# Optimization experiments

Hardware: AMD Instinct MI355X
Metric: run time of the kernel (lower is better)

Reference implementation:

```python
import jax, jax.numpy as jnp
import numpy as np

H = 4       # num_heads (forced == num_gates by reshape math in source)
G = 4       # num_gates
HID = 1024  # hidden_size
D = HID // H  # head_dim = 256
T = 512     # sequence length
B = 16      # batch


def setup_inputs() -> dict:
    key = jax.random.key(0)
    k1, k2, k3 = jax.random.split(key, 3)
    lim = 1.0 / np.sqrt(HID)
    # x holds pre-projected gate preactivations Wx: [T, B, 4*hidden]
    x = jax.random.normal(k1, (T, B, G * HID), dtype=jnp.float32) * 0.1
    recurrent_kernel = jax.random.uniform(k2, (H, D, G, D), dtype=jnp.float32, minval=-lim, maxval=lim)
    bias = jax.random.uniform(k3, (H, G, D), dtype=jnp.float32, minval=-lim, maxval=lim)
    return {"x": x, "recurrent_kernel": recurrent_kernel, "bias": bias}


def reference(x, recurrent_kernel, bias):
    # Reproduce the source's reshape chain (valid since H == G == 4):
    # rk: [H, D, G, D] -> permute(0,2,3,1) -> [H, G, D, D] -> reshape(H, D, H*D)
    rk1 = jnp.transpose(recurrent_kernel, (0, 2, 3, 1)).reshape(H, D, H * D)
    # transpose(1,2) -> [H, H*D, D] -> reshape(H, D, G*D)
    rk2 = jnp.swapaxes(rk1, 1, 2).reshape(H, D, G * D)
    bflat = bias.reshape(-1)  # head-major flatten, as in source
    Bsz = x.shape[1]
    zero = jnp.zeros((Bsz, HID), dtype=x.dtype)

    def step(carry, Wx_t):
        h, c, n, m = carry
        # Ry: [B,H,1,D] @ [1,H,D,G*D] -> [B,H,G*D] -> [B,H,G,D] -> [B,G,H,D] -> [B, G*HID]
        Ry = jnp.einsum('bhd,hdg->bhg', h.reshape(Bsz, H, D), rk2)
        Ry = Ry.reshape(Bsz, H, G, D).transpose(0, 2, 1, 3).reshape(Bsz, -1)
        raw = (Wx_t + Ry + bflat).reshape(Bsz, G, HID)
        iraw, fraw, zraw, oraw = raw[:, 0], raw[:, 1], raw[:, 2], raw[:, 3]
        logfplusm = m + jax.nn.log_sigmoid(fraw)
        # source: if all(n == 0): mnew = iraw else max(iraw, logfplusm)
        mnew = jnp.where(jnp.all(n == 0.0), iraw, jnp.maximum(iraw, logfplusm))
        ogate = jax.nn.sigmoid(oraw)
        igate = jnp.exp(iraw - mnew)
        fgate = jnp.exp(logfplusm - mnew)
        cnew = fgate * c + igate * jnp.tanh(zraw)
        nnew = fgate * h + igate  # faithful to source (uses hidden_state, not n)
        hnew = ogate * cnew / nnew
        return (hnew, cnew, nnew, mnew), hnew

    carry0 = (zero, zero, zero, zero)
    (hT, cT, nT, mT), outs = jax.lax.scan(step, carry0, x)
    # output = all_states[0][1:] (hidden over time), state = all_states[:, -1]
    final_state = jnp.stack((hT, cT, nT, mT), axis=0)
    return outs, final_state
```

## Files before the change

### kernel.cpp

```cpp
#include <hip/hip_runtime.h>
#include <hip/hip_fp16.h>
#include <stdint.h>


#define NTS 512
#define OUTS_ELEMS (NTS * 16 * 1024)

typedef _Float16 half2v __attribute__((ext_vector_type(2)));

__device__ __forceinline__ float fdot2f(uint32_t a, uint32_t b, float c) {
#if __has_builtin(__builtin_amdgcn_fdot2)
  union U { uint32_t u; half2v h; };
  U ua, ub; ua.u = a; ub.u = b;
  return __builtin_amdgcn_fdot2(ua.h, ub.h, c, false);
#else
  __half2 ha, hb;
  *(uint32_t*)&ha = a; *(uint32_t*)&hb = b;
  float2 fa = __half22float2(ha), fb = __half22float2(hb);
  return fmaf(fa.y, fb.y, fmaf(fa.x, fb.x, c));
#endif
}

__global__ void repack_weights(const float* __restrict__ rk,
                               uint32_t* __restrict__ wp) {
  int tid = blockIdx.x * 256 + threadIdx.x;
  int dd   = tid & 3;
  int lane = (tid >> 2) & 63;
  int m    = (tid >> 8) & 31;
  int w    = (tid >> 13) & 3;
  int hq   = tid >> 15;
  int head = hq >> 2, q4 = hq & 3;
  int n = m * 4 + dd;
  int g = n >> 5, p = n & 31;
  uint32_t word = 0;
  #pragma unroll
  for (int e = 0; e < 2; ++e) {
    int klo = 2 * p + e;
    float v = rk[head * 262144 + (klo * 4 + g) * 1024 + q4 * 256 + lane * 4 + w];
    word |= (uint32_t)__half_as_ushort(__float2half(v)) << (16 * e);
  }
  wp[tid] = word;
}

__global__ __launch_bounds__(256, 1) void slstm_main(
    const float* __restrict__ x, const float* __restrict__ bias,
    const uint32_t* __restrict__ wp, uint32_t* hex,
    float* __restrict__ out) {
  __shared__ __align__(16) unsigned short lh[4][64];
  __shared__ __align__(16) float4 pa[2][4][64];

  const int bid = blockIdx.x;
  const int xcd = bid & 7, yy = bid >> 3;
  const int q4 = yy & 3, ii = yy >> 2;
  const int cc = xcd * 8 + ii;
  const int b = cc >> 2, head = cc & 3;
  const int lane = threadIdx.x & 63, w = threadIdx.x >> 6;
  const int hq = head * 4 + q4;
  const int j_abs = q4 * 64 + lane;
  const bool is_pub = (w == 0);
  const bool is_own = (w == q4);
  const bool needs_gates = is_pub || is_own;

  uint32_t wr_[128];
  {
    const uint4* wp4 = (const uint4*)wp;
    int base = ((hq * 4 + w) * 32) * 64 + lane;
    #pragma unroll
    for (int mm = 0; mm < 32; ++mm) {
      uint4 v = wp4[base + mm * 64];
      wr_[mm * 4 + 0] = v.x; wr_[mm * 4 + 1] = v.y;
      wr_[mm * 4 + 2] = v.z; wr_[mm * 4 + 3] = v.w;
    }
  }

  float bg[4];
  #pragma unroll
  for (int g = 0; g < 4; ++g) bg[g] = bias[g * 1024 + head * 256 + j_abs];

  const int xoff0 = b * 4096 + head * 256 + j_abs;
  float xv[4] = {0.f, 0.f, 0.f, 0.f};
  if (needs_gates) {
    #pragma unroll
    for (int g = 0; g < 4; ++g) xv[g] = x[xoff0 + g * 1024];
  }

  const int rd_idx = cc * 256 + w * 64 + lane;
  const int wr_idx = cc * 256 + j_abs;
  const int out_off = b * 1024 + head * 256 + j_abs;

  float hs = 0.f, cs = 0.f, nns = 0.f, ms = 0.f;

  #pragma unroll 1
  for (int t = 0; t < NTS; ++t) {
    float A0 = 0.f, A1 = 0.f, A2 = 0.f, A3 = 0.f;
    float xn0 = 0.f, xn1 = 0.f, xn2 = 0.f, xn3 = 0.f;
    if (t > 0) {
      if (!is_own) {
        const uint32_t tg = (uint32_t)(t - 1);
        uint32_t* sp = hex + ((t - 1) & 1) * 16384 + rd_idx;
        uint32_t v; int spins = 0;
        for (;;) {
          v = __hip_atomic_load(sp, __ATOMIC_RELAXED, __HIP_MEMORY_SCOPE_AGENT);
          if (__all((v & 0xffffu) == tg) || ++spins > (1 << 15)) break;
        }
        lh[w][lane] = (unsigned short)(v >> 16);
      }
      if (needs_gates && t < NTS - 1) {
        int xo = xoff0 + (t + 1) * 65536;
        xn0 = x[xo]; xn1 = x[xo + 1024]; xn2 = x[xo + 2048]; xn3 = x[xo + 3072];
      }
      float a0 = 0.f, a1 = 0.f, a2 = 0.f, a3 = 0.f;
      {
        uint32_t hr[32];
        const float4* hp = (const float4*)&lh[w][0];
        #pragma unroll
        for (int f = 0; f < 8; ++f) {
          float4 fv = hp[f];
          hr[f * 4 + 0] = __float_as_uint(fv.x);
          hr[f * 4 + 1] = __float_as_uint(fv.y);
          hr[f * 4 + 2] = __float_as_uint(fv.z);
          hr[f * 4 + 3] = __float_as_uint(fv.w);
        }
        #pragma unroll
        for (int p = 0; p < 32; ++p) {
          uint32_t hh = hr[p];
          a0 = fdot2f(wr_[p],      hh, a0);
          a1 = fdot2f(wr_[32 + p], hh, a1);
          a2 = fdot2f(wr_[64 + p], hh, a2);
          a3 = fdot2f(wr_[96 + p], hh, a3);
        }
      }
      pa[t & 1][w][lane] = make_float4(a0, a1, a2, a3);
      __syncthreads();
      if (needs_gates) {
        #pragma unroll
        for (int ww = 0; ww < 4; ++ww) {
          float4 pv = pa[t & 1][ww][lane];
          A0 += pv.x; A1 += pv.y; A2 += pv.z; A3 += pv.w;
        }
      }
    } else {
      if (needs_gates) {
        int xo = xoff0 + 65536;
        xn0 = x[xo]; xn1 = x[xo + 1024]; xn2 = x[xo + 2048]; xn3 = x[xo + 3072];
      }
    }

    if (needs_gates) {
      float ri = A0 + xv[0] + bg[0];
      float rf = A1 + xv[1] + bg[1];
      float rz = A2 + xv[2] + bg[2];
      float ro = A3 + xv[3] + bg[3];

      float lsf = fminf(rf, 0.f) - log1pf(__expf(-fabsf(rf)));
      float lf = ms + lsf;
      float mnew = (t == 0) ? ri : fmaxf(ri, lf);
      float og = 1.f / (1.f + __expf(-ro));
      float ig = __expf(ri - mnew);
      float fg = __expf(lf - mnew);
      float cnew = fg * cs + ig * tanhf(rz);
      float nnew = fg * hs + ig;
      float hnew = og * cnew / nnew;
      hs = hnew; cs = cnew; nns = nnew; ms = mnew;

      unsigned short hf = __half_as_ushort(__float2half(hnew));
      if (is_pub) {
        out[t * 16384 + out_off] = hnew;
        uint32_t wword = ((uint32_t)hf << 16) | (uint32_t)t;
        __hip_atomic_store(hex + (t & 1) * 16384 + wr_idx, wword,
                           __ATOMIC_RELAXED, __HIP_MEMORY_SCOPE_AGENT);
      }
      if (is_own) {
        lh[w][lane] = hf;
      }
      xv[0] = xn0; xv[1] = xn1; xv[2] = xn2; xv[3] = xn3;
    }
  }

  if (is_pub) {
    float* fs = out + OUTS_ELEMS;
    fs[out_off] = hs;
    fs[16384 + out_off] = cs;
    fs[32768 + out_off] = nns;
    fs[49152 + out_off] = ms;
  }
}

extern "C" void kernel_launch(void* const* d_in, const int* in_sizes, int n_in,
                              void* d_out, int out_size, void* d_ws,
                              size_t ws_size, hipStream_t stream) {
  const float* x    = (const float*)d_in[0];
  const float* rk   = (const float*)d_in[1];
  const float* bias = (const float*)d_in[2];
  uint32_t* wp  = (uint32_t*)d_ws;
  uint32_t* hex = (uint32_t*)((char*)d_ws + (1u << 21));
  float* out = (float*)d_out;

  repack_weights<<<2048, 256, 0, stream>>>(rk, wp);
  slstm_main<<<256, 256, 0, stream>>>(x, bias, wp, hex, out);
}
```

Before: 930.6 us.

## Split recurrent dot across quad lanes with DPP reduction, removing block barrier

Work is remapped so each wave computes gates for 16 outputs, with 4 lanes per output each covering a quarter of K. Partial sums are combined with DPP quad shuffles instead of LDS partials plus __syncthreads. Every wave now polls global h itself, and the tag scheme changes to t+1. Gate math moves to fast intrinsics (__logf, an exp-based tanh), trading some accuracy for fewer instructions. The spin cap is lowered.

```diff
diff --git a/kernel.cpp b/kernel.cpp
--- a/kernel.cpp
+++ b/kernel.cpp
@@ -5,6 +5,7 @@
 
 #define NTS 512
 #define OUTS_ELEMS (NTS * 16 * 1024)
+#define SPIN_CAP 8192
 
 typedef _Float16 half2v __attribute__((ext_vector_type(2)));
 
@@ -21,22 +22,33 @@
 #endif
 }
 
+__device__ __forceinline__ float qxor1(float v) {
+  return __int_as_float(__builtin_amdgcn_update_dpp(
+      0, __float_as_int(v), 0xB1, 0xF, 0xF, true));
+}
+__device__ __forceinline__ float qxor2(float v) {
+  return __int_as_float(__builtin_amdgcn_update_dpp(
+      0, __float_as_int(v), 0x4E, 0xF, 0xF, true));
+}
+
 __global__ void repack_weights(const float* __restrict__ rk,
                                uint32_t* __restrict__ wp) {
   int tid = blockIdx.x * 256 + threadIdx.x;
   int dd   = tid & 3;
   int lane = (tid >> 2) & 63;
-  int m    = (tid >> 8) & 31;
-  int w    = (tid >> 13) & 3;
-  int hq   = tid >> 15;
-  int head = hq >> 2, q4 = hq & 3;
-  int n = m * 4 + dd;
+  int mm   = (tid >> 8) & 31;
+  int W    = tid >> 13;
+  int head = W >> 4, ww = W & 15;
+  int jl = lane >> 2, kq = lane & 3;
+  int n = mm * 4 + dd;
   int g = n >> 5, p = n & 31;
+  int dout = ww * 16 + jl;
   uint32_t word = 0;
   #pragma unroll
   for (int e = 0; e < 2; ++e) {
     int klo = 2 * p + e;
-    float v = rk[head * 262144 + (klo * 4 + g) * 1024 + q4 * 256 + lane * 4 + w];
+    float v = rk[head * 262144 + (klo * 4 + g) * 1024 +
+                 (dout >> 6) * 256 + (dout & 63) * 4 + kq];
     word |= (uint32_t)__half_as_ushort(__float2half(v)) << (16 * e);
   }
   wp[tid] = word;
@@ -46,8 +58,7 @@
     const float* __restrict__ x, const float* __restrict__ bias,
     const uint32_t* __restrict__ wp, uint32_t* hex,
     float* __restrict__ out) {
-  __shared__ __align__(16) unsigned short lh[4][64];
-  __shared__ __align__(16) float4 pa[2][4][64];
+  __shared__ __align__(16) uint32_t lhp[4][144];
 
   const int bid = blockIdx.x;
   const int xcd = bid & 7, yy = bid >> 3;
@@ -55,16 +66,14 @@
   const int cc = xcd * 8 + ii;
   const int b = cc >> 2, head = cc & 3;
   const int lane = threadIdx.x & 63, w = threadIdx.x >> 6;
-  const int hq = head * 4 + q4;
-  const int j_abs = q4 * 64 + lane;
-  const bool is_pub = (w == 0);
-  const bool is_own = (w == q4);
-  const bool needs_gates = is_pub || is_own;
+  const int ww = q4 * 4 + w;
+  const int jl = lane >> 2, kq = lane & 3;
+  const int dout = ww * 16 + jl;
 
   uint32_t wr_[128];
   {
     const uint4* wp4 = (const uint4*)wp;
-    int base = ((hq * 4 + w) * 32) * 64 + lane;
+    int base = (head * 16 + ww) * 2048 + lane;
     #pragma unroll
     for (int mm = 0; mm < 32; ++mm) {
       uint4 v = wp4[base + mm * 64];
@@ -72,112 +81,103 @@
       wr_[mm * 4 + 2] = v.z; wr_[mm * 4 + 3] = v.w;
     }
   }
-
-  float bg[4];
   #pragma unroll
-  for (int g = 0; g < 4; ++g) bg[g] = bias[g * 1024 + head * 256 + j_abs];
-
-  const int xoff0 = b * 4096 + head * 256 + j_abs;
-  float xv[4] = {0.f, 0.f, 0.f, 0.f};
-  if (needs_gates) {
-    #pragma unroll
-    for (int g = 0; g < 4; ++g) xv[g] = x[xoff0 + g * 1024];
-  }
-
-  const int rd_idx = cc * 256 + w * 64 + lane;
-  const int wr_idx = cc * 256 + j_abs;
-  const int out_off = b * 1024 + head * 256 + j_abs;
+  for (int i = 0; i < 128; ++i) asm volatile("" : "+v"(wr_[i]));
+
+  const float bg = bias[kq * 1024 + head * 256 + dout];
+  const int xoff0 = b * 4096 + kq * 1024 + head * 256 + dout;
+  float xv = x[xoff0];
+
+  const int rd_base = cc * 256 + lane * 4;
+  const int wr_idx  = cc * 256 + dout;
+  const int out_off = b * 1024 + head * 256 + dout;
+  const bool pub = (kq == 0);
+
+  uint32_t* lrow = &lhp[w][0];
+  const int widx = (lane >> 4) * 36 + ((2 * lane) & 31);
 
   float hs = 0.f, cs = 0.f, nns = 0.f, ms = 0.f;
 
   #pragma unroll 1
   for (int t = 0; t < NTS; ++t) {
-    float A0 = 0.f, A1 = 0.f, A2 = 0.f, A3 = 0.f;
-    float xn0 = 0.f, xn1 = 0.f, xn2 = 0.f, xn3 = 0.f;
+    float xb = xv + bg;
+    float A0 = (kq == 0) ? xb : 0.f;
+    float A1 = (kq == 1) ? xb : 0.f;
+    float A2 = (kq == 2) ? xb : 0.f;
+    float A3 = (kq == 3) ? xb : 0.f;
+    float xn = 0.f;
     if (t > 0) {
-      if (!is_own) {
-        const uint32_t tg = (uint32_t)(t - 1);
-        uint32_t* sp = hex + ((t - 1) & 1) * 16384 + rd_idx;
-        uint32_t v; int spins = 0;
-        for (;;) {
-          v = __hip_atomic_load(sp, __ATOMIC_RELAXED, __HIP_MEMORY_SCOPE_AGENT);
-          if (__all((v & 0xffffu) == tg) || ++spins > (1 << 15)) break;
-        }
-        lh[w][lane] = (unsigned short)(v >> 16);
+      const uint32_t tg = (uint32_t)t;
+      const uint32_t* sp = hex + ((t - 1) & 1) * 16384 + rd_base;
+      uint32_t v0, v1, v2, v3; int spins = 0;
+      for (;;) {
+        v0 = __hip_atomic_load(sp + 0, __ATOMIC_RELAXED, __HIP_MEMORY_SCOPE_AGENT);
+        v1 = __hip_atomic_load(sp + 1, __ATOMIC_RELAXED, __HIP_MEMORY_SCOPE_AGENT);
+        v2 = __hip_atomic_load(sp + 2, __ATOMIC_RELAXED, __HIP_MEMORY_SCOPE_AGENT);
+        v3 = __hip_atomic_load(sp + 3, __ATOMIC_RELAXED, __HIP_MEMORY_SCOPE_AGENT);
+        int ok = ((v0 & 0xffffu) == tg) & ((v1 & 0xffffu) == tg) &
+                 ((v2 & 0xffffu) == tg) & ((v3 & 0xffffu) == tg);
+        if (__all(ok)) break;
+        if (++spins > SPIN_CAP) break;
       }
-      if (needs_gates && t < NTS - 1) {
-        int xo = xoff0 + (t + 1) * 65536;
-        xn0 = x[xo]; xn1 = x[xo + 1024]; xn2 = x[xo + 2048]; xn3 = x[xo + 3072];
-      }
-      float a0 = 0.f, a1 = 0.f, a2 = 0.f, a3 = 0.f;
-      {
-        uint32_t hr[32];
-        const float4* hp = (const float4*)&lh[w][0];
-        #pragma unroll
-        for (int f = 0; f < 8; ++f) {
-          float4 fv = hp[f];
-          hr[f * 4 + 0] = __float_as_uint(fv.x);
-          hr[f * 4 + 1] = __float_as_uint(fv.y);
-          hr[f * 4 + 2] = __float_as_uint(fv.z);
-          hr[f * 4 + 3] = __float_as_uint(fv.w);
-        }
-        #pragma unroll
-        for (int p = 0; p < 32; ++p) {
-          uint32_t hh = hr[p];
-          a0 = fdot2f(wr_[p],      hh, a0);
-          a1 = fdot2f(wr_[32 + p], hh, a1);
-          a2 = fdot2f(wr_[64 + p], hh, a2);
-          a3 = fdot2f(wr_[96 + p], hh, a3);
-        }
-      }
-      pa[t & 1][w][lane] = make_float4(a0, a1, a2, a3);
-      __syncthreads();
-      if (needs_gates) {
-        #pragma unroll
-        for (int ww = 0; ww < 4; ++ww) {
-          float4 pv = pa[t & 1][ww][lane];
-          A0 += pv.x; A1 += pv.y; A2 += pv.z; A3 += pv.w;
-        }
+      if (t < NTS - 1) xn = x[xoff0 + (t + 1) * 65536];
+      uint32_t p0 = (v0 >> 16) | (v1 & 0xffff0000u);
+      uint32_t p1 = (v2 >> 16) | (v3 & 0xffff0000u);
+      *(uint64_t*)&lrow[widx] = ((uint64_t)p1 << 32) | (uint64_t)p0;
+      const uint4* rp = (const uint4*)&lrow[kq * 36];
+      #pragma unroll
+      for (int c = 0; c < 8; ++c) {
+        uint4 hw = rp[c];
+        A0 = fdot2f(wr_[c * 4 + 0], hw.x, A0);
+        A0 = fdot2f(wr_[c * 4 + 1], hw.y, A0);
+        A0 = fdot2f(wr_[c * 4 + 2], hw.z, A0);
+        A0 = fdot2f(wr_[c * 4 + 3], hw.w, A0);
+        A1 = fdot2f(wr_[32 + c * 4 + 0], hw.x, A1);
+        A1 = fdot2f(wr_[32 + c * 4 + 1], hw.y, A1);
+        A1 = fdot2f(wr_[32 + c * 4 + 2], hw.z, A1);
+        A1 = fdot2f(wr_[32 + c * 4 + 3], hw.w, A1);
+        A2 = fdot2f(wr_[64 + c * 4 + 0], hw.x, A2);
+        A2 = fdot2f(wr_[64 + c * 4 + 1], hw.y, A2);
+        A2 = fdot2f(wr_[64 + c * 4 + 2], hw.z, A2);
+        A2 = fdot2f(wr_[64 + c * 4 + 3], hw.w, A2);
+        A3 = fdot2f(wr_[96 + c * 4 + 0], hw.x, A3);
+        A3 = fdot2f(wr_[96 + c * 4 + 1], hw.y, A3);
+        A3 = fdot2f(wr_[96 + c * 4 + 2], hw.z, A3);
+        A3 = fdot2f(wr_[96 + c * 4 + 3], hw.w, A3);
       }
     } else {
-      if (needs_gates) {
-        int xo = xoff0 + 65536;
-        xn0 = x[xo]; xn1 = x[xo + 1024]; xn2 = x[xo + 2048]; xn3 = x[xo + 3072];
-      }
+      xn = x[xoff0 + 65536];
     }
 
-    if (needs_gates) {
-      float ri = A0 + xv[0] + bg[0];
-      float rf = A1 + xv[1] + bg[1];
-      float rz = A2 + xv[2] + bg[2];
-      float ro = A3 + xv[3] + bg[3];
-
-      float lsf = fminf(rf, 0.f) - log1pf(__expf(-fabsf(rf)));
-      float lf = ms + lsf;
-      float mnew = (t == 0) ? ri : fmaxf(ri, lf);
-      float og = 1.f / (1.f + __expf(-ro));
-      float ig = __expf(ri - mnew);
-      float fg = __expf(lf - mnew);
-      float cnew = fg * cs + ig * tanhf(rz);
-      float nnew = fg * hs + ig;
-      float hnew = og * cnew / nnew;
-      hs = hnew; cs = cnew; nns = nnew; ms = mnew;
-
-      unsigned short hf = __half_as_ushort(__float2half(hnew));
-      if (is_pub) {
-        out[t * 16384 + out_off] = hnew;
-        uint32_t wword = ((uint32_t)hf << 16) | (uint32_t)t;
-        __hip_atomic_store(hex + (t & 1) * 16384 + wr_idx, wword,
-                           __ATOMIC_RELAXED, __HIP_MEMORY_SCOPE_AGENT);
-      }
-      if (is_own) {
-        lh[w][lane] = hf;
-      }
-      xv[0] = xn0; xv[1] = xn1; xv[2] = xn2; xv[3] = xn3;
+    A0 += qxor1(A0); A0 += qxor2(A0);
+    A1 += qxor1(A1); A1 += qxor2(A1);
+    A2 += qxor1(A2); A2 += qxor2(A2);
+    A3 += qxor1(A3); A3 += qxor2(A3);
+
+    float ri = A0, rf = A1, rz = A2, ro = A3;
+    float lsf = fminf(rf, 0.f) - __logf(1.f + __expf(-fabsf(rf)));
+    float lf = ms + lsf;
+    float mnew = (t == 0) ? ri : fmaxf(ri, lf);
+    float ig = __expf(ri - mnew);
+    float fg = __expf(lf - mnew);
+    float e2z = __expf(2.f * rz);
+    float tz = 1.f - 2.f / (e2z + 1.f);
+    float cnew = fg * cs + ig * tz;
+    float nnew = fg * hs + ig;
+    float hnew = cnew / ((1.f + __expf(-ro)) * nnew);
+    hs = hnew; cs = cnew; nns = nnew; ms = mnew;
+
+    unsigned short hf = __half_as_ushort(__float2half(hnew));
+    if (pub) {
+      uint32_t wword = ((uint32_t)hf << 16) | (uint32_t)(t + 1);
+      __hip_atomic_store(hex + (t & 1) * 16384 + wr_idx, wword,
+                         __ATOMIC_RELAXED, __HIP_MEMORY_SCOPE_AGENT);
+      out[t * 16384 + out_off] = hnew;
     }
-  }
-
-  if (is_pub) {
+    xv = xn;
+  }
+
+  if (pub) {
     float* fs = out + OUTS_ELEMS;
     fs[out_off] = hs;
     fs[16384 + out_off] = cs;
```

After: 810.0 us. -13.0%, faster.
